# Performance work log

Hardware: AMD Instinct MI355X
Metric: run time of the kernel (lower is better)

Reference implementation:

```python
import jax, jax.numpy as jnp
import numpy as np

TEMPERATURE = 8.0  # sqrt(head_dim=64)
NEG_FILL = -1000000000.0

def setup_inputs() -> dict:
    key = jax.random.key(0)
    k1, k2, k3, k4, k5 = jax.random.split(key, 5)
    B, H, S, D = 4, 16, 1024, 64
    q = jax.random.normal(k1, (B, H, S, D), dtype=jnp.float32)
    k = jax.random.normal(k2, (B, H, S, D), dtype=jnp.float32)
    v = jax.random.normal(k3, (B, H, S, D), dtype=jnp.float32)
    similarity = jax.random.normal(k4, (B, H, S, S), dtype=jnp.float32)
    mask = jax.random.randint(k5, (B, 1, S, S), 0, 2).astype(bool)
    return {"q": q, "k": k, "v": v, "similarity": similarity, "mask": mask}

def reference(q, k, v, similarity, mask):
    # scores: [B,H,S,S] = (q/temp) @ k^T
    attn = jnp.einsum('bhqd,bhkd->bhqk', q / TEMPERATURE, k)
    attn = jnp.where(mask, NEG_FILL, attn)          # masked_fill (mask broadcasts over heads)
    attn = jax.nn.softmax(attn + similarity, axis=-1)  # dropout p=0 (eval): identity
    output = jnp.einsum('bhqk,bhkd->bhqd', attn, v)
    return (output, attn)
```

## Files before the change

### kernel.cpp

```cpp
#include <hip/hip_runtime.h>
#include <stdint.h>


#define S_LEN 1024
#define D_DIM 64
#define QT 16
#define NEG_FILL (-1000000000.0f)
#define LOG2E 1.44269504088896340736f

typedef __bf16 bf16x8 __attribute__((ext_vector_type(8)));
typedef float f32x4 __attribute__((ext_vector_type(4)));
typedef unsigned short u16x4 __attribute__((ext_vector_type(4)));
typedef unsigned short u16x8 __attribute__((ext_vector_type(8)));

__device__ __forceinline__ unsigned short f2bf(float x) {
    unsigned u = __builtin_bit_cast(unsigned, x);
    u += 0x7fffu + ((u >> 16) & 1u);
    return (unsigned short)(u >> 16);
}
__device__ __forceinline__ float bf2f(unsigned short b) {
    return __builtin_bit_cast(float, (unsigned)b << 16);
}

__global__ void prep_qk(const float* __restrict__ q, const float* __restrict__ k,
                        unsigned short* __restrict__ Qb, unsigned short* __restrict__ Kb)
{
    int i = blockIdx.x * 256 + threadIdx.x;
    f32x4 q4 = ((const f32x4*)q)[i];
    f32x4 k4 = ((const f32x4*)k)[i];
    u16x4 qo, ko;
#pragma unroll
    for (int j = 0; j < 4; ++j) {
        qo[j] = f2bf(q4[j] * 0.125f);
        ko[j] = f2bf(k4[j]);
    }
    ((u16x4*)Qb)[i] = qo;
    ((u16x4*)Kb)[i] = ko;
}

__global__ void prep_vt(const float* __restrict__ v, unsigned short* __restrict__ Vt)
{
    __shared__ unsigned short sT[64 * 72];
    const int bh = blockIdx.x >> 4;
    const int st = blockIdx.x & 15;
    const int t = threadIdx.x;
    const float* vb = v + (size_t)(bh * S_LEN + st * 64) * D_DIM;
#pragma unroll
    for (int p = 0; p < 4; ++p) {
        int lin = p * 256 + t;
        int r = lin >> 4;
        int c = lin & 15;
        f32x4 x = ((const f32x4*)(vb + r * D_DIM))[c];
        unsigned short* dst = &sT[r * 72 + c * 4];
#pragma unroll
        for (int j = 0; j < 4; ++j) dst[j] = f2bf(x[j]);
    }
    __syncthreads();
    unsigned short* ob = Vt + (size_t)bh * D_DIM * S_LEN + st * 64;
#pragma unroll
    for (int p = 0; p < 4; ++p) {
        int lin = p * 256 + t;
        int d = lin >> 4;
        int s4 = (lin & 15) * 4;
        u16x4 o;
#pragma unroll
        for (int j = 0; j < 4; ++j) o[j] = sT[(s4 + j) * 72 + d];
        *(u16x4*)&ob[d * S_LEN + s4] = o;
    }
}

__global__ void prep_mask(const void* __restrict__ mraw, unsigned char* __restrict__ Mb)
{
    __shared__ int s_not_int, s_not_f32;
    const int t = threadIdx.x;
    if (t == 0) { s_not_int = 0; s_not_f32 = 0; }
    __syncthreads();
    const unsigned* w = (const unsigned*)mraw;
    int ni = 0, nf = 0;
    for (int j = t; j < 1024; j += 256) {
        unsigned x = w[j];
        if (x > 1u) ni = 1;
        if (x != 0u && x != 0x3f800000u) nf = 1;
    }
    if (ni) s_not_int = 1;
    if (nf) s_not_f32 = 1;
    __syncthreads();
    const int fmt = (s_not_int == 0) ? 0 : ((s_not_f32 == 0) ? 1 : 2);
    const int i = blockIdx.x * 256 + t;
    uchar4 o;
    if (fmt == 0) {
        int4 x = ((const int4*)mraw)[i];
        o.x = x.x ? 1 : 0; o.y = x.y ? 1 : 0; o.z = x.z ? 1 : 0; o.w = x.w ? 1 : 0;
    } else if (fmt == 1) {
        float4 x = ((const float4*)mraw)[i];
        o.x = (x.x != 0.f) ? 1 : 0; o.y = (x.y != 0.f) ? 1 : 0;
        o.z = (x.z != 0.f) ? 1 : 0; o.w = (x.w != 0.f) ? 1 : 0;
    } else {
        uchar4 x = ((const uchar4*)mraw)[i];
        o.x = x.x ? 1 : 0; o.y = x.y ? 1 : 0; o.z = x.z ? 1 : 0; o.w = x.w ? 1 : 0;
    }
    ((uchar4*)Mb)[i] = o;
}

__global__ __launch_bounds__(256, 3)
void attn_main(const float* __restrict__ simg_, const unsigned short* __restrict__ Qb,
               const unsigned short* __restrict__ Kb, const unsigned short* __restrict__ Vtb,
               const unsigned char* __restrict__ Mb, float* __restrict__ out,
               float* __restrict__ attn)
{
    __shared__ __align__(16) unsigned short sQ[QT * 72];
    __shared__ __align__(16) unsigned short sKV[64 * 72];
    __shared__ __align__(16) unsigned short sS[QT * (S_LEN + 8)];

    const int blk = blockIdx.x;
    const int bh = blk >> 6;
    const int qt = blk & 63;
    const int b = bh >> 4;
    const int t = threadIdx.x;
    const int w = t >> 6;
    const int lane = t & 63;
    const int quad = lane >> 4;
    const int l15 = lane & 15;

    const unsigned short* Qg = Qb + (size_t)(bh * S_LEN + qt * QT) * D_DIM;
    const unsigned short* Kg = Kb + (size_t)bh * S_LEN * D_DIM;
    const unsigned short* Vg = Vtb + (size_t)bh * D_DIM * S_LEN;
    const float* simg = simg_ + ((size_t)(bh * S_LEN + qt * QT)) * S_LEN;
    const unsigned char* mg = Mb + ((size_t)(b * S_LEN + qt * QT)) * S_LEN;
    float* attng = attn + ((size_t)(bh * S_LEN + qt * QT)) * S_LEN;

    if (t < 128) {
        int r = t >> 3, c = t & 7;
        *(u16x8*)&sQ[r * 72 + c * 8] = *(const u16x8*)&Qg[r * D_DIM + c * 8];
    }

    const int n0 = w * 16;
    for (int kt = 0; kt < 16; ++kt) {
        __syncthreads();
#pragma unroll
        for (int c = 0; c < 2; ++c) {
            int lin = c * 256 + t;
            int r = lin >> 3, ch = lin & 7;
            *(u16x8*)&sKV[r * 72 + ch * 8] =
                *(const u16x8*)&Kg[(size_t)(kt * 64 + r) * D_DIM + ch * 8];
        }
        __syncthreads();
        f32x4 acc = {0.f, 0.f, 0.f, 0.f};
#pragma unroll
        for (int kk = 0; kk < 2; ++kk) {
            bf16x8 av = *(const bf16x8*)&sQ[l15 * 72 + kk * 32 + quad * 8];
            bf16x8 bv = *(const bf16x8*)&sKV[(n0 + l15) * 72 + kk * 32 + quad * 8];
            acc = __builtin_amdgcn_mfma_f32_16x16x32_bf16(av, bv, acc, 0, 0, 0);
        }
        const int colg = kt * 64 + n0 + l15;
#pragma unroll
        for (int r = 0; r < 4; ++r) {
            int row = quad * 4 + r;
            float s = acc[r];
            float sv = simg[row * S_LEN + colg];
            unsigned char mk = mg[row * S_LEN + colg];
            s = (mk ? NEG_FILL : s) + sv;
            sS[row * (S_LEN + 8) + colg] = f2bf(s);
        }
    }
    __syncthreads();

#pragma unroll 1
    for (int rr = 0; rr < 4; ++rr) {
        const int row = w * 4 + rr;
        float vals[16];
        float mx = -3.0e38f;
#pragma unroll
        for (int j = 0; j < 4; ++j) {
            int col = j * 256 + lane * 4;
            u16x4 x = *(const u16x4*)&sS[row * (S_LEN + 8) + col];
#pragma unroll
            for (int i = 0; i < 4; ++i) {
                float f = bf2f(x[i]);
                vals[j * 4 + i] = f;
                mx = fmaxf(mx, f);
            }
        }
#pragma unroll
        for (int off = 32; off > 0; off >>= 1)
            mx = fmaxf(mx, __shfl_xor(mx, off, 64));
        float sum = 0.f;
#pragma unroll
        for (int i = 0; i < 16; ++i) {
            float e = exp2f((vals[i] - mx) * LOG2E);
            vals[i] = e;
            sum += e;
        }
#pragma unroll
        for (int off = 32; off > 0; off >>= 1)
            sum += __shfl_xor(sum, off, 64);
        const float rinv = 1.0f / sum;
#pragma unroll
        for (int j = 0; j < 4; ++j) {
            int col = j * 256 + lane * 4;
            f32x4 p;
            u16x4 pb;
#pragma unroll
            for (int i = 0; i < 4; ++i) {
                float pi = vals[j * 4 + i] * rinv;
                p[i] = pi;
                pb[i] = f2bf(pi);
            }
            *(f32x4*)&attng[row * S_LEN + col] = p;
            *(u16x4*)&sS[row * (S_LEN + 8) + col] = pb;
        }
    }

    f32x4 oacc = {0.f, 0.f, 0.f, 0.f};
    const int d0 = w * 16;
    for (int kt = 0; kt < 16; ++kt) {
        __syncthreads();
#pragma unroll
        for (int c = 0; c < 2; ++c) {
            int lin = c * 256 + t;
            int r = lin >> 3, ch = lin & 7;
            *(u16x8*)&sKV[r * 72 + ch * 8] =
                *(const u16x8*)&Vg[(size_t)r * S_LEN + kt * 64 + ch * 8];
        }
        __syncthreads();
#pragma unroll
        for (int kk = 0; kk < 2; ++kk) {
            bf16x8 av = *(const bf16x8*)&sS[l15 * (S_LEN + 8) + kt * 64 + kk * 32 + quad * 8];
            bf16x8 bv = *(const bf16x8*)&sKV[(d0 + l15) * 72 + kk * 32 + quad * 8];
            oacc = __builtin_amdgcn_mfma_f32_16x16x32_bf16(av, bv, oacc, 0, 0, 0);
        }
    }
    float* og = out + ((size_t)(bh * S_LEN + qt * QT)) * D_DIM;
#pragma unroll
    for (int r = 0; r < 4; ++r) {
        int row = quad * 4 + r;
        og[row * D_DIM + d0 + l15] = oacc[r];
    }
}

extern "C" void kernel_launch(void* const* d_in, const int* in_sizes, int n_in,
                              void* d_out, int out_size, void* d_ws, size_t ws_size,
                              hipStream_t stream)
{
    const float* q = (const float*)d_in[0];
    const float* k = (const float*)d_in[1];
    const float* v = (const float*)d_in[2];
    const float* sim = (const float*)d_in[3];
    const void* mask = d_in[4];
    float* out = (float*)d_out;
    float* attn = out + (size_t)4 * 16 * 1024 * 64;

    char* ws = (char*)d_ws;
    unsigned short* Qb = (unsigned short*)(ws + (size_t)0);
    unsigned short* Kb = (unsigned short*)(ws + ((size_t)8 << 20));
    unsigned short* Vt = (unsigned short*)(ws + ((size_t)16 << 20));
    unsigned char*  Mb = (unsigned char*)(ws + ((size_t)24 << 20));

    prep_qk<<<4096, 256, 0, stream>>>(q, k, Qb, Kb);
    prep_vt<<<1024, 256, 0, stream>>>(v, Vt);
    prep_mask<<<4096, 256, 0, stream>>>(mask, Mb);
    attn_main<<<4096, 256, 0, stream>>>(sim, Qb, Kb, Vt, Mb, out, attn);
}
```

Measured before the change: 632.6 us.

## Load K/V fragments directly from global, coalesce sim/mask reads, fuse prep kernels

The main kernel drops the shared-memory staging of Q, K and V and their per-tile barriers, loading MFMA operands straight from global or L2. The similarity and mask reads move from the scattered per-MFMA-fragment pattern into the softmax pass, where each lane reads contiguous float4 and uchar4 vectors. Occupancy in launch bounds rises from 3 to 4, and the qk and mask prep kernels are fused into one launch. The risk is more uncoalesced global traffic for K/V fragments, which relies on cache hits. The mask is now applied after the bf16 rounding of scores, which slightly changes where rounding happens.

Measured after the change: 575.8 us. 9.0% less time.

```diff
diff --git a/kernel.cpp b/kernel.cpp
--- a/kernel.cpp
+++ b/kernel.cpp
@@ -5,6 +5,7 @@
 #define S_LEN 1024
 #define D_DIM 64
 #define QT 16
+#define SSTR 1032
 #define NEG_FILL (-1000000000.0f)
 #define LOG2E 1.44269504088896340736f
 
@@ -22,10 +23,13 @@
     return __builtin_bit_cast(float, (unsigned)b << 16);
 }
 
-__global__ void prep_qk(const float* __restrict__ q, const float* __restrict__ k,
-                        unsigned short* __restrict__ Qb, unsigned short* __restrict__ Kb)
-{
-    int i = blockIdx.x * 256 + threadIdx.x;
+__global__ void prep_qkm(const float* __restrict__ q, const float* __restrict__ k,
+                         const void* __restrict__ mraw,
+                         unsigned short* __restrict__ Qb, unsigned short* __restrict__ Kb,
+                         unsigned char* __restrict__ Mb)
+{
+    const int t = threadIdx.x;
+    const int i = blockIdx.x * 256 + t;
     f32x4 q4 = ((const f32x4*)q)[i];
     f32x4 k4 = ((const f32x4*)k)[i];
     u16x4 qo, ko;
@@ -36,49 +40,14 @@
     }
     ((u16x4*)Qb)[i] = qo;
     ((u16x4*)Kb)[i] = ko;
-}
-
-__global__ void prep_vt(const float* __restrict__ v, unsigned short* __restrict__ Vt)
-{
-    __shared__ unsigned short sT[64 * 72];
-    const int bh = blockIdx.x >> 4;
-    const int st = blockIdx.x & 15;
-    const int t = threadIdx.x;
-    const float* vb = v + (size_t)(bh * S_LEN + st * 64) * D_DIM;
-#pragma unroll
-    for (int p = 0; p < 4; ++p) {
-        int lin = p * 256 + t;
-        int r = lin >> 4;
-        int c = lin & 15;
-        f32x4 x = ((const f32x4*)(vb + r * D_DIM))[c];
-        unsigned short* dst = &sT[r * 72 + c * 4];
-#pragma unroll
-        for (int j = 0; j < 4; ++j) dst[j] = f2bf(x[j]);
-    }
-    __syncthreads();
-    unsigned short* ob = Vt + (size_t)bh * D_DIM * S_LEN + st * 64;
-#pragma unroll
-    for (int p = 0; p < 4; ++p) {
-        int lin = p * 256 + t;
-        int d = lin >> 4;
-        int s4 = (lin & 15) * 4;
-        u16x4 o;
-#pragma unroll
-        for (int j = 0; j < 4; ++j) o[j] = sT[(s4 + j) * 72 + d];
-        *(u16x4*)&ob[d * S_LEN + s4] = o;
-    }
-}
-
-__global__ void prep_mask(const void* __restrict__ mraw, unsigned char* __restrict__ Mb)
-{
+
     __shared__ int s_not_int, s_not_f32;
-    const int t = threadIdx.x;
     if (t == 0) { s_not_int = 0; s_not_f32 = 0; }
     __syncthreads();
-    const unsigned* w = (const unsigned*)mraw;
+    const unsigned* wdd = (const unsigned*)mraw;
     int ni = 0, nf = 0;
     for (int j = t; j < 1024; j += 256) {
-        unsigned x = w[j];
+        unsigned x = wdd[j];
         if (x > 1u) ni = 1;
         if (x != 0u && x != 0x3f800000u) nf = 1;
     }
@@ -86,7 +55,6 @@
     if (nf) s_not_f32 = 1;
     __syncthreads();
     const int fmt = (s_not_int == 0) ? 0 : ((s_not_f32 == 0) ? 1 : 2);
-    const int i = blockIdx.x * 256 + t;
     uchar4 o;
     if (fmt == 0) {
         int4 x = ((const int4*)mraw)[i];
@@ -102,15 +70,44 @@
     ((uchar4*)Mb)[i] = o;
 }
 
-__global__ __launch_bounds__(256, 3)
+__global__ void prep_vt(const float* __restrict__ v, unsigned short* __restrict__ Vt)
+{
+    __shared__ unsigned short sT[64 * 72];
+    const int bh = blockIdx.x >> 4;
+    const int st = blockIdx.x & 15;
+    const int t = threadIdx.x;
+    const float* vb = v + (size_t)(bh * S_LEN + st * 64) * D_DIM;
+#pragma unroll
+    for (int p = 0; p < 4; ++p) {
+        int lin = p * 256 + t;
+        int r = lin >> 4;
+        int c = lin & 15;
+        f32x4 x = ((const f32x4*)(vb + r * D_DIM))[c];
+        unsigned short* dst = &sT[r * 72 + c * 4];
+#pragma unroll
+        for (int j = 0; j < 4; ++j) dst[j] = f2bf(x[j]);
+    }
+    __syncthreads();
+    unsigned short* ob = Vt + (size_t)bh * D_DIM * S_LEN + st * 64;
+#pragma unroll
+    for (int p = 0; p < 4; ++p) {
+        int lin = p * 256 + t;
+        int d = lin >> 4;
+        int s4 = (lin & 15) * 4;
+        u16x4 o;
+#pragma unroll
+        for (int j = 0; j < 4; ++j) o[j] = sT[(s4 + j) * 72 + d];
+        *(u16x4*)&ob[d * S_LEN + s4] = o;
+    }
+}
+
+__global__ __launch_bounds__(256, 4)
 void attn_main(const float* __restrict__ simg_, const unsigned short* __restrict__ Qb,
                const unsigned short* __restrict__ Kb, const unsigned short* __restrict__ Vtb,
                const unsigned char* __restrict__ Mb, float* __restrict__ out,
                float* __restrict__ attn)
 {
-    __shared__ __align__(16) unsigned short sQ[QT * 72];
-    __shared__ __align__(16) unsigned short sKV[64 * 72];
-    __shared__ __align__(16) unsigned short sS[QT * (S_LEN + 8)];
+    __shared__ __align__(16) unsigned short sS[QT * SSTR];
 
     const int blk = blockIdx.x;
     const int bh = blk >> 6;
@@ -129,57 +126,44 @@
     const unsigned char* mg = Mb + ((size_t)(b * S_LEN + qt * QT)) * S_LEN;
     float* attng = attn + ((size_t)(bh * S_LEN + qt * QT)) * S_LEN;
 
-    if (t < 128) {
-        int r = t >> 3, c = t & 7;
-        *(u16x8*)&sQ[r * 72 + c * 8] = *(const u16x8*)&Qg[r * D_DIM + c * 8];
-    }
-
     const int n0 = w * 16;
+    const bf16x8 av0 = *(const bf16x8*)&Qg[l15 * D_DIM + quad * 8];
+    const bf16x8 av1 = *(const bf16x8*)&Qg[l15 * D_DIM + 32 + quad * 8];
+#pragma unroll 4
     for (int kt = 0; kt < 16; ++kt) {
-        __syncthreads();
-#pragma unroll
-        for (int c = 0; c < 2; ++c) {
-            int lin = c * 256 + t;
-            int r = lin >> 3, ch = lin & 7;
-            *(u16x8*)&sKV[r * 72 + ch * 8] =
-                *(const u16x8*)&Kg[(size_t)(kt * 64 + r) * D_DIM + ch * 8];
-        }
-        __syncthreads();
+        const unsigned short* kp = &Kg[(size_t)(kt * 64 + n0 + l15) * D_DIM + quad * 8];
+        bf16x8 bv0 = *(const bf16x8*)kp;
+        bf16x8 bv1 = *(const bf16x8*)(kp + 32);
         f32x4 acc = {0.f, 0.f, 0.f, 0.f};
-#pragma unroll
-        for (int kk = 0; kk < 2; ++kk) {
-            bf16x8 av = *(const bf16x8*)&sQ[l15 * 72 + kk * 32 + quad * 8];
-            bf16x8 bv = *(const bf16x8*)&sKV[(n0 + l15) * 72 + kk * 32 + quad * 8];
-            acc = __builtin_amdgcn_mfma_f32_16x16x32_bf16(av, bv, acc, 0, 0, 0);
-        }
+        acc = __builtin_amdgcn_mfma_f32_16x16x32_bf16(av0, bv0, acc, 0, 0, 0);
+        acc = __builtin_amdgcn_mfma_f32_16x16x32_bf16(av1, bv1, acc, 0, 0, 0);
         const int colg = kt * 64 + n0 + l15;
 #pragma unroll
-        for (int r = 0; r < 4; ++r) {
-            int row = quad * 4 + r;
-            float s = acc[r];
-            float sv = simg[row * S_LEN + colg];
-            unsigned char mk = mg[row * S_LEN + colg];
-            s = (mk ? NEG_FILL : s) + sv;
-            sS[row * (S_LEN + 8) + colg] = f2bf(s);
-        }
+        for (int r = 0; r < 4; ++r)
+            sS[(quad * 4 + r) * SSTR + colg] = f2bf(acc[r]);
     }
     __syncthreads();
 
 #pragma unroll 1
     for (int rr = 0; rr < 4; ++rr) {
         const int row = w * 4 + rr;
+        const float* sp = simg + (size_t)row * S_LEN;
+        const unsigned char* mp = mg + (size_t)row * S_LEN;
         float vals[16];
         float mx = -3.0e38f;
 #pragma unroll
         for (int j = 0; j < 4; ++j) {
             int col = j * 256 + lane * 4;
-            u16x4 x = *(const u16x4*)&sS[row * (S_LEN + 8) + col];
-#pragma unroll
-            for (int i = 0; i < 4; ++i) {
-                float f = bf2f(x[i]);
-                vals[j * 4 + i] = f;
-                mx = fmaxf(mx, f);
-            }
+            u16x4 x = *(const u16x4*)&sS[row * SSTR + col];
+            f32x4 sv = *(const f32x4*)&sp[col];
+            uchar4 mk = *(const uchar4*)&mp[col];
+            float f0 = mk.x ? NEG_FILL : (bf2f(x[0]) + sv[0]);
+            float f1 = mk.y ? NEG_FILL : (bf2f(x[1]) + sv[1]);
+            float f2 = mk.z ? NEG_FILL : (bf2f(x[2]) + sv[2]);
+            float f3 = mk.w ? NEG_FILL : (bf2f(x[3]) + sv[3]);
+            vals[j * 4 + 0] = f0; vals[j * 4 + 1] = f1;
+            vals[j * 4 + 2] = f2; vals[j * 4 + 3] = f3;
+            mx = fmaxf(mx, fmaxf(fmaxf(f0, f1), fmaxf(f2, f3)));
         }
 #pragma unroll
         for (int off = 32; off > 0; off >>= 1)
@@ -206,29 +190,23 @@
                 p[i] = pi;
                 pb[i] = f2bf(pi);
             }
-            *(f32x4*)&attng[row * S_LEN + col] = p;
-            *(u16x4*)&sS[row * (S_LEN + 8) + col] = pb;
+            *(f32x4*)&attng[(size_t)row * S_LEN + col] = p;
+            *(u16x4*)&sS[row * SSTR + col] = pb;
         }
     }
+    __syncthreads();
 
     f32x4 oacc = {0.f, 0.f, 0.f, 0.f};
     const int d0 = w * 16;
+#pragma unroll 4
     for (int kt = 0; kt < 16; ++kt) {
-        __syncthreads();
-#pragma unroll
-        for (int c = 0; c < 2; ++c) {
-            int lin = c * 256 + t;
-            int r = lin >> 3, ch = lin & 7;
-            *(u16x8*)&sKV[r * 72 + ch * 8] =
-                *(const u16x8*)&Vg[(size_t)r * S_LEN + kt * 64 + ch * 8];
-        }
-        __syncthreads();
-#pragma unroll
-        for (int kk = 0; kk < 2; ++kk) {
-            bf16x8 av = *(const bf16x8*)&sS[l15 * (S_LEN + 8) + kt * 64 + kk * 32 + quad * 8];
-            bf16x8 bv = *(const bf16x8*)&sKV[(d0 + l15) * 72 + kk * 32 + quad * 8];
-            oacc = __builtin_amdgcn_mfma_f32_16x16x32_bf16(av, bv, oacc, 0, 0, 0);
-        }
+        const unsigned short* vp = &Vg[(size_t)(d0 + l15) * S_LEN + kt * 64 + quad * 8];
+        bf16x8 bv0 = *(const bf16x8*)vp;
+        bf16x8 bv1 = *(const bf16x8*)(vp + 32);
+        bf16x8 pa0 = *(const bf16x8*)&sS[l15 * SSTR + kt * 64 + quad * 8];
+        bf16x8 pa1 = *(const bf16x8*)&sS[l15 * SSTR + kt * 64 + 32 + quad * 8];
+        oacc = __builtin_amdgcn_mfma_f32_16x16x32_bf16(pa0, bv0, oacc, 0, 0, 0);
+        oacc = __builtin_amdgcn_mfma_f32_16x16x32_bf16(pa1, bv1, oacc, 0, 0, 0);
     }
     float* og = out + ((size_t)(bh * S_LEN + qt * QT)) * D_DIM;
 #pragma unroll
@@ -256,8 +234,7 @@
     unsigned short* Vt = (unsigned short*)(ws + ((size_t)16 << 20));
     unsigned char*  Mb = (unsigned char*)(ws + ((size_t)24 << 20));
 
-    prep_qk<<<4096, 256, 0, stream>>>(q, k, Qb, Kb);
+    prep_qkm<<<4096, 256, 0, stream>>>(q, k, mask, Qb, Kb, Mb);
     prep_vt<<<1024, 256, 0, stream>>>(v, Vt);
-    prep_mask<<<4096, 256, 0, stream>>>(mask, Mb);
     attn_main<<<4096, 256, 0, stream>>>(sim, Qb, Kb, Vt, Mb, out, attn);
 }
```
